# Kernel optimization log

Hardware: AMD Instinct MI355X
Metric: run time of the kernel (lower is better)

## Reference

```python
import jax, jax.numpy as jnp
from jax import lax
import numpy as np

KEY = 4
WIDTH = 32
CH = 3


def _inv_perm():
    # Reproduce construct_mapping(4, 32, 3): mapping[0] = arange(384),
    # mapping[1] = blocks of a (4,32,3) index grid split into 4x4x3 column
    # blocks, flattened. tensor_map does out[:, perm] = in[:, arange], i.e.
    # a scatter; equivalently out = in[:, argsort(perm)].
    s = np.arange(KEY * WIDTH * CH).reshape(KEY, WIDTH, CH)
    perm = np.concatenate([s[:, j:j + KEY, :].reshape(-1) for j in range(0, WIDTH, KEY)])
    return np.argsort(perm)  # (384,)

_INV = jnp.asarray(_inv_perm())


def _conv(x, w, b):
    y = lax.conv_general_dilated(x, w, (1, 1), 'SAME',
                                 dimension_numbers=('NCHW', 'OIHW', 'NCHW'))
    return y + b[None, :, None, None]


def _maxpool2(x):
    return lax.reduce_window(x, -jnp.inf, lax.max,
                             (1, 1, 2, 2), (1, 1, 2, 2), 'VALID')


def setup_inputs() -> dict:
    key = jax.random.key(0)
    ks = jax.random.split(key, 10)
    f32 = jnp.float32
    B = 8192
    return {
        'x': jax.random.normal(ks[0], (B, 32, 32, 3), dtype=f32),
        'W_lin': jax.random.normal(ks[1], (48, 48), dtype=f32) * 0.1,
        'conv1_w': jax.random.normal(ks[2], (32, 3, 3, 3), dtype=f32) * 0.1,
        'conv1_b': jax.random.normal(ks[3], (32,), dtype=f32) * 0.05,
        'conv2_w': jax.random.normal(ks[4], (64, 32, 3, 3), dtype=f32) * 0.05,
        'conv2_b': jax.random.normal(ks[5], (64,), dtype=f32) * 0.05,
        'conv3_w': jax.random.normal(ks[6], (128, 64, 3, 3), dtype=f32) * 0.05,
        'conv3_b': jax.random.normal(ks[7], (128,), dtype=f32) * 0.05,
        'fc_w': jax.random.normal(ks[8], (10, 2048), dtype=f32) * 0.02,
        'fc_b': jax.random.normal(ks[9], (10,), dtype=f32) * 0.02,
        'stage': 2,
    }


def reference(x, W_lin, conv1_w, conv1_b, conv2_w, conv2_b, conv3_w, conv3_b,
              fc_w, fc_b, stage):
    B = x.shape[0]
    if stage == 2:
        # 64 blocks of 4x4x3 in row-major block order (i outer, j inner).
        xb = x.reshape(B, 8, KEY, 8, KEY, CH)            # (B, ib, ir, jb, jc, c)
        xb = xb.transpose(0, 1, 3, 2, 4, 5).reshape(B, 64, 48)
        y = jnp.einsum('bnk,ok->bno', xb, W_lin)          # per-block linear (no bias)
        # group 8 column-blocks per row-block -> (B, 8, 384), permute columns
        y = y.reshape(B, 8, 384)[:, :, _INV]
        x_final = y.reshape(B, 32, 32, 3).transpose(0, 3, 1, 2)  # NCHW
    else:
        x_final = x
    h = _maxpool2(jax.nn.relu(_conv(x_final, conv1_w, conv1_b)))
    h = _maxpool2(jax.nn.relu(_conv(h, conv2_w, conv2_b)))
    h = _maxpool2(jax.nn.relu(_conv(h, conv3_w, conv3_b)))
    h = h.reshape(-1, 2048)
    logits = h @ fc_w.T + fc_b
    return jax.nn.log_softmax(logits, axis=-1)
```

## Files before the change

### kernel.cpp

```cpp
#include <hip/hip_runtime.h>
#include <hip/hip_bf16.h>

typedef unsigned short u16;
typedef __attribute__((ext_vector_type(8))) short short8v;
typedef __attribute__((ext_vector_type(4))) float f32x4;
typedef __attribute__((ext_vector_type(16))) float f32x16;
typedef union { short8v v; uint u[4]; } pack8;

__device__ __forceinline__ float bu2f(u16 u) {
    return __uint_as_float(((unsigned)u) << 16);
}
__device__ __forceinline__ u16 f2bu(float f) {
    unsigned u = __float_as_uint(f);
    u += 0x7fffu + ((u >> 16) & 1u);
    return (u16)(u >> 16);
}
__device__ __forceinline__ uint pk2(float a, float b) {
    return (uint)f2bu(a) | ((uint)f2bu(b) << 16);
}

__global__ __launch_bounds__(256) void k_repack(
    const float* __restrict__ Wlin, const float* __restrict__ c1w,
    const float* __restrict__ c2w, const float* __restrict__ c3w,
    u16* __restrict__ w1p, u16* __restrict__ s2wp,
    u16* __restrict__ w2p, u16* __restrict__ w3p)
{
    int i = blockIdx.x * 256 + threadIdx.x;
    if (i < 32 * 48) {
        int oc = i / 48, k = i - oc * 48;
        int kh = k >> 4, e = k & 15;
        int kw = e >> 2, c = e & 3;
        u16 v = 0;
        if (kw < 3 && c < 3)
            v = f2bu(c1w[((oc * 3 + c) * 3 + kh) * 3 + kw]);
        w1p[i] = v;
    }
    if (i < 96 * 72) {
        int r = i / 72, k = i - r * 72;
        u16 v = 0;
        if (k < 48) {
            int o = r % 48;
            float w = Wlin[o * 48 + k];
            u16 hi = f2bu(w);
            v = (r < 48) ? hi : f2bu(w - bu2f(hi));
        }
        s2wp[i] = v;
    }
    if (i < 64 * 288) {
        int oc = i / 288, r = i - oc * 288;
        int tap = r >> 5, ic = r & 31;
        w2p[oc * 296 + r] = f2bu(c2w[(oc * 32 + ic) * 9 + tap]);
    }
    if (i < 128 * 576) {
        int oc = i / 576, r = i - oc * 576;
        int tap = r >> 6, ic = r & 63;
        w3p[oc * 584 + r] = f2bu(c3w[(oc * 64 + ic) * 9 + tap]);
    }
}

#define IMG4  0
#define XB    4624
#define IN3   0
#define IN2   6400
#define XF    6400
#define LDS_N 19360

__global__ __launch_bounds__(256, 4) void k_img(
    const float* __restrict__ x, const u16* __restrict__ s2wp,
    const u16* __restrict__ w1p, const float* __restrict__ c1b,
    const int* __restrict__ stage,
    const u16* __restrict__ w2p, const float* __restrict__ c2b,
    const u16* __restrict__ w3p, const float* __restrict__ c3b,
    const float* __restrict__ fw, const float* __restrict__ fb,
    float* __restrict__ out)
{
    __shared__ __align__(16) u16 lds[LDS_N];
    const int b = blockIdx.x, t = threadIdx.x;
    const int wv = t >> 6, lane = t & 63, lr = lane & 15, q = lane >> 4;
    const int oc32 = lane & 31, hi = lane >> 5;
    uint* z32 = (uint*)lds;

    for (int i = t; i < 2312; i += 256) z32[i] = 0u;
    short8v wb1[3];
    #pragma unroll
    for (int s = 0; s < 3; ++s)
        wb1[s] = *(const short8v*)(&w1p[oc32 * 48 + s * 16 + hi * 8]);

    const int sv = stage[0];
    if (sv == 2) {
        {
            const int n = t >> 2, ir = t & 3;
            const float* xp = x + (size_t)b * 3072 + (((n >> 3) * 4 + ir) * 96 + (n & 7) * 12);
            const float4 va = ((const float4*)xp)[0];
            const float4 vb = ((const float4*)xp)[1];
            const float4 vc = ((const float4*)xp)[2];
            uint* dst = (uint*)&lds[XB + n * 72 + ir * 12];
            dst[0] = pk2(va.x, va.y); dst[1] = pk2(va.z, va.w);
            dst[2] = pk2(vb.x, vb.y); dst[3] = pk2(vb.z, vb.w);
            dst[4] = pk2(vc.x, vc.y); dst[5] = pk2(vc.z, vc.w);
            if (ir < 2) {
                uint* z2 = (uint*)&lds[XB + n * 72 + 48 + ir * 8];
                z2[0] = 0u; z2[1] = 0u; z2[2] = 0u; z2[3] = 0u;
            }
        }
        short8v bh0[3], bh1[3], bl0[3], bl1[3];
        #pragma unroll
        for (int nf = 0; nf < 3; ++nf) {
            bh0[nf] = *(const short8v*)(&s2wp[(nf * 16 + lr) * 72 + q * 8]);
            bh1[nf] = *(const short8v*)(&s2wp[(nf * 16 + lr) * 72 + 32 + q * 8]);
            bl0[nf] = *(const short8v*)(&s2wp[(48 + nf * 16 + lr) * 72 + q * 8]);
            bl1[nf] = *(const short8v*)(&s2wp[(48 + nf * 16 + lr) * 72 + 32 + q * 8]);
        }
        __syncthreads();
        short8v a0 = *(const short8v*)&lds[XB + (wv * 16 + lr) * 72 + q * 8];
        short8v a1 = *(const short8v*)&lds[XB + (wv * 16 + lr) * 72 + 32 + q * 8];
        f32x4 y[3];
        #pragma unroll
        for (int nf = 0; nf < 3; ++nf) {
            y[nf] = (f32x4){0.f, 0.f, 0.f, 0.f};
            y[nf] = __builtin_amdgcn_mfma_f32_16x16x32_bf16(a0, bh0[nf], y[nf], 0, 0, 0);
            y[nf] = __builtin_amdgcn_mfma_f32_16x16x32_bf16(a1, bh1[nf], y[nf], 0, 0, 0);
            y[nf] = __builtin_amdgcn_mfma_f32_16x16x32_bf16(a0, bl0[nf], y[nf], 0, 0, 0);
            y[nf] = __builtin_amdgcn_mfma_f32_16x16x32_bf16(a1, bl1[nf], y[nf], 0, 0, 0);
        }
        __syncthreads();
        #pragma unroll
        for (int nf = 0; nf < 3; ++nf)
            #pragma unroll
            for (int r = 0; r < 4; ++r) {
                int n2 = wv * 16 + q * 4 + r;
                int o  = nf * 16 + lr;
                int ir = o / 12, rm = o - ir * 12;
                int jc = rm / 3, c = rm - jc * 3;
                int hh = (n2 >> 3) * 4 + ir, ww = (n2 & 7) * 4 + jc;
                lds[IMG4 + ((hh + 1) * 34 + (ww + 1)) * 4 + c] = f2bu(y[nf][r]);
            }
    } else {
        if (t < 4) z32[2312 + t] = 0u;
        __syncthreads();
        for (int e = t; e < 3072; e += 256) {
            int hh = e / 96, rm = e - hh * 96;
            int ww = rm / 3, c = rm - ww * 3;
            lds[IMG4 + ((hh + 1) * 34 + (ww + 1)) * 4 + c] = f2bu(x[(size_t)b * 3072 + e]);
        }
    }
    __syncthreads();

    for (int i = t; i < 1360; i += 256) {
        int cell = i / 20, d = i - cell * 20;
        int h, w;
        if (cell < 18)      { h = 0;  w = cell; }
        else if (cell < 36) { h = 17; w = cell - 18; }
        else { int k = cell - 36; h = 1 + (k >> 1); w = (k & 1) * 17; }
        z32[3200 + (h * 18 + w) * 20 + d] = 0u;
    }
    {
        const float bias1 = c1b[oc32];
        #pragma unroll
        for (int chk = 0; chk < 4; ++chk) {
            f32x16 acc0, acc1;
            #pragma unroll
            for (int i = 0; i < 16; ++i) { acc0[i] = 0.f; acc1[i] = 0.f; }
            #pragma unroll
            for (int s = 0; s < 3; ++s) {
                #pragma unroll
                for (int f = 0; f < 2; ++f) {
                    const int h = wv * 8 + chk * 2 + f;
                    const int a4 = ((h + s) * 34 + oc32 + hi * 2) * 4;
                    pack8 pk;
                    *(unsigned long long*)&pk.u[0] = *(const unsigned long long*)(&lds[IMG4 + a4]);
                    *(unsigned long long*)&pk.u[2] = *(const unsigned long long*)(&lds[IMG4 + a4 + 4]);
                    if (f == 0) acc0 = __builtin_amdgcn_mfma_f32_32x32x16_bf16(pk.v, wb1[s], acc0, 0, 0, 0);
                    else        acc1 = __builtin_amdgcn_mfma_f32_32x32x16_bf16(pk.v, wb1[s], acc1, 0, 0, 0);
                }
            }
            const int hq = wv * 4 + chk;
            #pragma unroll
            for (int g = 0; g < 4; ++g) {
                #pragma unroll
                for (int pp = 0; pp < 2; ++pp) {
                    const int i0 = 4 * g + 2 * pp;
                    float m0 = fmaxf(acc0[i0], acc0[i0 + 1]);
                    float m1 = fmaxf(acc1[i0], acc1[i0 + 1]);
                    float v = fmaxf(fmaxf(m0, m1) + bias1, 0.f);
                    const int wq = 4 * g + 2 * hi + pp;
                    lds[IN2 + ((hq + 1) * 18 + (wq + 1)) * 40 + oc32] = f2bu(v);
                }
            }
        }
    }
    __syncthreads();

    for (int i = t; i < 1152; i += 256) {
        int cell = i >> 5, d = i & 31;
        int pos;
        if (cell < 10)      pos = cell;
        else if (cell < 20) pos = 90 + (cell - 10);
        else { int k = cell - 20; pos = (1 + (k >> 1)) * 10 + (k & 1) * 9; }
        z32[pos * 32 + d] = 0u;
    }
    #pragma unroll
    for (int nh = 0; nh < 2; ++nh) {
        const u16* wb2 = w2p + (size_t)(nh * 32 + lr) * 296 + q * 8;
        f32x4 acc[4][2];
        #pragma unroll
        for (int m = 0; m < 4; ++m)
            #pragma unroll
            for (int n = 0; n < 2; ++n) acc[m][n] = (f32x4){0.f, 0.f, 0.f, 0.f};

        short8v bfr[3][2];
        #pragma unroll
        for (int n = 0; n < 2; ++n) {
            bfr[0][n] = *(const short8v*)(wb2 + n * 4736 + 0);
            bfr[1][n] = *(const short8v*)(wb2 + n * 4736 + 32);
        }
        #pragma unroll
        for (int s = 0; s < 9; ++s) {
            if (s + 2 < 9) {
                #pragma unroll
                for (int n = 0; n < 2; ++n)
                    bfr[(s + 2) % 3][n] = *(const short8v*)(wb2 + n * 4736 + (s + 2) * 32);
            }
            const int kh = s / 3, kw = s - kh * 3;
            short8v af[4];
            #pragma unroll
            for (int m = 0; m < 4; ++m)
                af[m] = *(const short8v*)(&lds[IN2 + ((wv * 4 + m + kh) * 18 + lr + kw) * 40 + q * 8]);
            __builtin_amdgcn_s_setprio(1);
            #pragma unroll
            for (int m = 0; m < 4; ++m)
                #pragma unroll
                for (int n = 0; n < 2; ++n)
                    acc[m][n] = __builtin_amdgcn_mfma_f32_16x16x32_bf16(af[m], bfr[s % 3][n], acc[m][n], 0, 0, 0);
            __builtin_amdgcn_s_setprio(0);
        }
        #pragma unroll
        for (int n = 0; n < 2; ++n) {
            float bias = c2b[nh * 32 + n * 16 + lr];
            #pragma unroll
            for (int mp = 0; mp < 2; ++mp) {
                #pragma unroll
                for (int p = 0; p < 2; ++p) {
                    float m0 = fmaxf(acc[2 * mp][n][2 * p], acc[2 * mp][n][2 * p + 1]);
                    float m1 = fmaxf(acc[2 * mp + 1][n][2 * p], acc[2 * mp + 1][n][2 * p + 1]);
                    float v = fmaxf(fmaxf(m0, m1) + bias, 0.f);
                    int hq = wv * 2 + mp, wq = 2 * q + p;
                    int posW = (hq + 1) * 10 + (wq + 1);
                    int oc = nh * 32 + n * 16 + lr;
                    lds[IN3 + posW * 64 + (oc ^ ((posW & 7) << 3))] = f2bu(v);
                }
            }
        }
    }
    __syncthreads();

    {
        const int ocb = wv * 32;
        const int hA = lr >> 3, wA = lr & 7;
        const u16* wb3 = w3p + (size_t)(ocb + lr) * 584 + q * 8;

        f32x4 acc3[4][2];
        #pragma unroll
        for (int m = 0; m < 4; ++m)
            #pragma unroll
            for (int n = 0; n < 2; ++n) acc3[m][n] = (f32x4){0.f, 0.f, 0.f, 0.f};

        short8v br[3][2];
        #pragma unroll
        for (int n = 0; n < 2; ++n) {
            br[0][n] = *(const short8v*)(wb3 + n * 9344 + 0);
            br[1][n] = *(const short8v*)(wb3 + n * 9344 + 32);
        }
        #pragma unroll
        for (int s = 0; s < 18; ++s) {
            if (s + 2 < 18) {
                const int off2 = ((s + 2) >> 1) * 64 + ((s + 2) & 1) * 32;
                #pragma unroll
                for (int n = 0; n < 2; ++n)
                    br[(s + 2) % 3][n] = *(const short8v*)(wb3 + n * 9344 + off2);
            }
            const int tap = s >> 1, half = s & 1;
            const int kh = tap / 3, kw = tap - kh * 3;
            short8v a3[4];
            #pragma unroll
            for (int m = 0; m < 4; ++m) {
                int posR = (m * 2 + hA + kh) * 10 + wA + kw;
                int sl = (half * 32 + q * 8) ^ ((posR & 7) << 3);
                a3[m] = *(const short8v*)(&lds[IN3 + posR * 64 + sl]);
            }
            __builtin_amdgcn_s_setprio(1);
            #pragma unroll
            for (int m = 0; m < 4; ++m)
                #pragma unroll
                for (int n = 0; n < 2; ++n)
                    acc3[m][n] = __builtin_amdgcn_mfma_f32_16x16x32_bf16(a3[m], br[s % 3][n], acc3[m][n], 0, 0, 0);
            __builtin_amdgcn_s_setprio(0);
        }
        #pragma unroll
        for (int n = 0; n < 2; ++n) {
            float bias = c3b[ocb + n * 16 + lr];
            #pragma unroll
            for (int m = 0; m < 4; ++m) {
                #pragma unroll
                for (int p = 0; p < 2; ++p) {
                    float mm = fmaxf(acc3[m][n][2 * p], acc3[m][n][2 * p + 1]);
                    float v2 = fmaxf(mm, __shfl_xor(mm, 32));
                    float v = fmaxf(v2 + bias, 0.f);
                    if (lane < 32) {
                        int wq = (q & 1) * 2 + p;
                        lds[XF + (ocb + n * 16 + lr) * 16 + m * 4 + wq] = f2bu(v);
                    }
                }
            }
        }
    }
    __syncthreads();

    {
        const short8v xv = *(const short8v*)(&lds[XF + t * 8]);
        float xr[8];
        #pragma unroll
        for (int i = 0; i < 8; ++i) xr[i] = bu2f(((const u16*)&xv)[i]);
        float part[10];
        #pragma unroll
        for (int o = 0; o < 10; ++o) {
            const float* wr = fw + (size_t)o * 2048 + t * 8;
            const float4 wa = ((const float4*)wr)[0];
            const float4 wb = ((const float4*)wr)[1];
            part[o] = xr[0] * wa.x + xr[1] * wa.y + xr[2] * wa.z + xr[3] * wa.w
                    + xr[4] * wb.x + xr[5] * wb.y + xr[6] * wb.z + xr[7] * wb.w;
        }
        #pragma unroll
        for (int o = 0; o < 10; ++o) {
            float s = part[o];
            #pragma unroll
            for (int d = 32; d > 0; d >>= 1) s += __shfl_xor(s, d);
            part[o] = s;
        }
        float* redf = (float*)&lds[XF + 2048];
        if (lane == 0) {
            #pragma unroll
            for (int o = 0; o < 10; ++o) redf[wv * 10 + o] = part[o];
        }
        __syncthreads();
        if (wv == 0) {
            float lg = -1e30f;
            if (lane < 10)
                lg = redf[lane] + redf[10 + lane] + redf[20 + lane] + redf[30 + lane] + fb[lane];
            float mx = lg;
            #pragma unroll
            for (int d = 8; d > 0; d >>= 1) mx = fmaxf(mx, __shfl_xor(mx, d));
            float ex = (lane < 10) ? expf(lg - mx) : 0.f;
            float den = ex;
            #pragma unroll
            for (int d = 8; d > 0; d >>= 1) den += __shfl_xor(den, d);
            if (lane < 10)
                out[(size_t)b * 10 + lane] = lg - mx - logf(den);
        }
    }
}

extern "C" void kernel_launch(void* const* d_in, const int* in_sizes, int n_in,
                              void* d_out, int out_size, void* d_ws, size_t ws_size,
                              hipStream_t stream)
{
    const float* x    = (const float*)d_in[0];
    const float* Wlin = (const float*)d_in[1];
    const float* c1w  = (const float*)d_in[2];
    const float* c1b  = (const float*)d_in[3];
    const float* c2w  = (const float*)d_in[4];
    const float* c2b  = (const float*)d_in[5];
    const float* c3w  = (const float*)d_in[6];
    const float* c3b  = (const float*)d_in[7];
    const float* fw   = (const float*)d_in[8];
    const float* fb   = (const float*)d_in[9];
    const int* stage  = (const int*)d_in[10];
    float* out = (float*)d_out;

    const int B = in_sizes[0] / 3072;

    char* ws = (char*)d_ws;
    u16* w1p  = (u16*)(ws);
    u16* s2wp = (u16*)(ws + 4608);
    u16* w2p  = (u16*)(ws + 18432);
    u16* w3p  = (u16*)(ws + 56320);

    k_repack<<<288, 256, 0, stream>>>(Wlin, c1w, c2w, c3w, w1p, s2wp, w2p, w3p);
    k_img   <<<B, 256, 0, stream>>>(x, s2wp, w1p, c1b, stage, w2p, c2b, w3p, c3b, fw, fb, out);
}
```

Before: 238.7 us.

## Shrink LDS footprint by overlapping conv2 input with image and buffering conv2 outputs in registers

```diff
diff --git a/kernel.cpp b/kernel.cpp
--- a/kernel.cpp
+++ b/kernel.cpp
@@ -61,9 +61,8 @@
 #define IMG4  0
 #define XB    4624
 #define IN3   0
-#define IN2   6400
-#define XF    6400
-#define LDS_N 19360
+#define IN2   4624
+#define LDS_N 16288
 
 __global__ __launch_bounds__(256, 4) void k_img(
     const float* __restrict__ x, const u16* __restrict__ s2wp,
@@ -146,13 +145,13 @@
     }
     __syncthreads();
 
-    for (int i = t; i < 1360; i += 256) {
-        int cell = i / 20, d = i - cell * 20;
+    for (int i = t; i < 1224; i += 256) {
+        int cell = i / 18, d = i - cell * 18;
         int h, w;
         if (cell < 18)      { h = 0;  w = cell; }
         else if (cell < 36) { h = 17; w = cell - 18; }
         else { int k = cell - 36; h = 1 + (k >> 1); w = (k & 1) * 17; }
-        z32[3200 + (h * 18 + w) * 20 + d] = 0u;
+        z32[2312 + (h * 18 + w) * 18 + d] = 0u;
     }
     {
         const float bias1 = c1b[oc32];
@@ -184,7 +183,59 @@
                     float m1 = fmaxf(acc1[i0], acc1[i0 + 1]);
                     float v = fmaxf(fmaxf(m0, m1) + bias1, 0.f);
                     const int wq = 4 * g + 2 * hi + pp;
-                    lds[IN2 + ((hq + 1) * 18 + (wq + 1)) * 40 + oc32] = f2bu(v);
+                    lds[IN2 + ((hq + 1) * 18 + (wq + 1)) * 36 + oc32] = f2bu(v);
+                }
+            }
+        }
+    }
+    __syncthreads();
+
+    float poo[16];
+    #pragma unroll
+    for (int nh = 0; nh < 2; ++nh) {
+        const u16* wb2 = w2p + (size_t)(nh * 32 + lr) * 296 + q * 8;
+        f32x4 acc[4][2];
+        #pragma unroll
+        for (int m = 0; m < 4; ++m)
+            #pragma unroll
+            for (int n = 0; n < 2; ++n) acc[m][n] = (f32x4){0.f, 0.f, 0.f, 0.f};
+
+        short8v bfr[3][2];
+        #pragma unroll
+        for (int n = 0; n < 2; ++n) {
+            bfr[0][n] = *(const short8v*)(wb2 + n * 4736 + 0);
+            bfr[1][n] = *(const short8v*)(wb2 + n * 4736 + 32);
+        }
+        #pragma unroll
+        for (int s = 0; s < 9; ++s) {
+            if (s + 2 < 9) {
+                #pragma unroll
+                for (int n = 0; n < 2; ++n)
+                    bfr[(s + 2) % 3][n] = *(const short8v*)(wb2 + n * 4736 + (s + 2) * 32);
+            }
+            const int kh = s / 3, kw = s - kh * 3;
+            short8v af[4];
+            #pragma unroll
+            for (int m = 0; m < 4; ++m)
+                af[m] = *(const short8v*)(&lds[IN2 + ((wv * 4 + m + kh) * 18 + lr + kw) * 36 + q * 8]);
+            __builtin_amdgcn_s_setprio(1);
+            #pragma unroll
+            for (int m = 0; m < 4; ++m)
+                #pragma unroll
+                for (int n = 0; n < 2; ++n)
+                    acc[m][n] = __builtin_amdgcn_mfma_f32_16x16x32_bf16(af[m], bfr[s % 3][n], acc[m][n], 0, 0, 0);
+            __builtin_amdgcn_s_setprio(0);
+        }
+        #pragma unroll
+        for (int n = 0; n < 2; ++n) {
+            float bias = c2b[nh * 32 + n * 16 + lr];
+            #pragma unroll
+            for (int mp = 0; mp < 2; ++mp) {
+                #pragma unroll
+                for (int p = 0; p < 2; ++p) {
+                    float m0 = fmaxf(acc[2 * mp][n][2 * p], acc[2 * mp][n][2 * p + 1]);
+                    float m1 = fmaxf(acc[2 * mp + 1][n][2 * p], acc[2 * mp + 1][n][2 * p + 1]);
+                    poo[nh * 8 + n * 4 + mp * 2 + p] = fmaxf(fmaxf(m0, m1) + bias, 0.f);
                 }
             }
         }
@@ -200,58 +251,19 @@
         z32[pos * 32 + d] = 0u;
     }
     #pragma unroll
-    for (int nh = 0; nh < 2; ++nh) {
-        const u16* wb2 = w2p + (size_t)(nh * 32 + lr) * 296 + q * 8;
-        f32x4 acc[4][2];
-        #pragma unroll
-        for (int m = 0; m < 4; ++m)
-            #pragma unroll
-            for (int n = 0; n < 2; ++n) acc[m][n] = (f32x4){0.f, 0.f, 0.f, 0.f};
-
-        short8v bfr[3][2];
-        #pragma unroll
-        for (int n = 0; n < 2; ++n) {
-            bfr[0][n] = *(const short8v*)(wb2 + n * 4736 + 0);
-            bfr[1][n] = *(const short8v*)(wb2 + n * 4736 + 32);
-        }
-        #pragma unroll
-        for (int s = 0; s < 9; ++s) {
-            if (s + 2 < 9) {
-                #pragma unroll
-                for (int n = 0; n < 2; ++n)
-                    bfr[(s + 2) % 3][n] = *(const short8v*)(wb2 + n * 4736 + (s + 2) * 32);
-            }
-            const int kh = s / 3, kw = s - kh * 3;
-            short8v af[4];
-            #pragma unroll
-            for (int m = 0; m < 4; ++m)
-                af[m] = *(const short8v*)(&lds[IN2 + ((wv * 4 + m + kh) * 18 + lr + kw) * 40 + q * 8]);
-            __builtin_amdgcn_s_setprio(1);
-            #pragma unroll
-            for (int m = 0; m < 4; ++m)
-                #pragma unroll
-                for (int n = 0; n < 2; ++n)
-                    acc[m][n] = __builtin_amdgcn_mfma_f32_16x16x32_bf16(af[m], bfr[s % 3][n], acc[m][n], 0, 0, 0);
-            __builtin_amdgcn_s_setprio(0);
-        }
-        #pragma unroll
-        for (int n = 0; n < 2; ++n) {
-            float bias = c2b[nh * 32 + n * 16 + lr];
-            #pragma unroll
-            for (int mp = 0; mp < 2; ++mp) {
+    for (int nh = 0; nh < 2; ++nh)
+        #pragma unroll
+        for (int n = 0; n < 2; ++n)
+            #pragma unroll
+            for (int mp = 0; mp < 2; ++mp)
                 #pragma unroll
                 for (int p = 0; p < 2; ++p) {
-                    float m0 = fmaxf(acc[2 * mp][n][2 * p], acc[2 * mp][n][2 * p + 1]);
-                    float m1 = fmaxf(acc[2 * mp + 1][n][2 * p], acc[2 * mp + 1][n][2 * p + 1]);
-                    float v = fmaxf(fmaxf(m0, m1) + bias, 0.f);
                     int hq = wv * 2 + mp, wq = 2 * q + p;
                     int posW = (hq + 1) * 10 + (wq + 1);
                     int oc = nh * 32 + n * 16 + lr;
-                    lds[IN3 + posW * 64 + (oc ^ ((posW & 7) << 3))] = f2bu(v);
+                    lds[IN3 + posW * 64 + (oc ^ ((posW & 7) << 3))] =
+                        f2bu(poo[nh * 8 + n * 4 + mp * 2 + p]);
                 }
-            }
-        }
-    }
     __syncthreads();
 
     {
@@ -296,6 +308,7 @@
                     acc3[m][n] = __builtin_amdgcn_mfma_f32_16x16x32_bf16(a3[m], br[s % 3][n], acc3[m][n], 0, 0, 0);
             __builtin_amdgcn_s_setprio(0);
         }
+        float* xff = (float*)lds;
         #pragma unroll
         for (int n = 0; n < 2; ++n) {
             float bias = c3b[ocb + n * 16 + lr];
@@ -308,7 +321,7 @@
                     float v = fmaxf(v2 + bias, 0.f);
                     if (lane < 32) {
                         int wq = (q & 1) * 2 + p;
-                        lds[XF + (ocb + n * 16 + lr) * 16 + m * 4 + wq] = f2bu(v);
+                        xff[3200 + (ocb + n * 16 + lr) * 16 + m * 4 + wq] = v;
                     }
                 }
             }
@@ -317,18 +330,17 @@
     __syncthreads();
 
     {
-        const short8v xv = *(const short8v*)(&lds[XF + t * 8]);
-        float xr[8];
-        #pragma unroll
-        for (int i = 0; i < 8; ++i) xr[i] = bu2f(((const u16*)&xv)[i]);
+        const float* xf = (const float*)lds + 3200;
+        const float4 xa = *(const float4*)(xf + t * 8);
+        const float4 xc = *(const float4*)(xf + t * 8 + 4);
         float part[10];
         #pragma unroll
         for (int o = 0; o < 10; ++o) {
             const float* wr = fw + (size_t)o * 2048 + t * 8;
             const float4 wa = ((const float4*)wr)[0];
             const float4 wb = ((const float4*)wr)[1];
-            part[o] = xr[0] * wa.x + xr[1] * wa.y + xr[2] * wa.z + xr[3] * wa.w
-                    + xr[4] * wb.x + xr[5] * wb.y + xr[6] * wb.z + xr[7] * wb.w;
+            part[o] = xa.x * wa.x + xa.y * wa.y + xa.z * wa.z + xa.w * wa.w
+                    + xc.x * wb.x + xc.y * wb.y + xc.z * wb.z + xc.w * wb.w;
         }
         #pragma unroll
         for (int o = 0; o < 10; ++o) {
@@ -337,7 +349,7 @@
             for (int d = 32; d > 0; d >>= 1) s += __shfl_xor(s, d);
             part[o] = s;
         }
-        float* redf = (float*)&lds[XF + 2048];
+        float* redf = (float*)lds + 5248;
         if (lane == 0) {
             #pragma unroll
             for (int o = 0; o < 10; ++o) redf[wv * 10 + o] = part[o];
```

New measurement: 238.2 us, median of 2. No clear change (-0.2%).
